# Kernel tuning notes

Hardware: AMD Instinct MI355X
Metric: run time of the kernel (lower is better)

Reference implementation:

```python
import jax, jax.numpy as jnp
import numpy as np

THRESH = 0.5
IOU_THR = 0.3
TOP_K = 512

# standard YOLOv3 anchors for strides 32/16/8 (grids 13/26/52)
ANCHORS_13 = jnp.array([[116., 90.], [156., 198.], [373., 326.]], dtype=jnp.float32)
ANCHORS_26 = jnp.array([[30., 61.], [62., 45.], [59., 119.]], dtype=jnp.float32)
ANCHORS_52 = jnp.array([[10., 13.], [16., 30.], [33., 23.]], dtype=jnp.float32)


def _decode(out, stride, anchors):
    # out: [B, 3*(5+C), H, W] -> [B, H, W, 3, 5+C] (matches permute(0,2,3,1).reshape)
    B, _, H, W = out.shape
    o = jnp.transpose(out, (0, 2, 3, 1)).reshape(B, H, W, 3, -1)
    conf = jax.nn.sigmoid(o[..., 4])          # [B,H,W,3]
    xy = jax.nn.sigmoid(o[..., 0:2])          # sigmoid on x,y as in _filter
    gy = jnp.arange(H, dtype=o.dtype)[None, :, None, None]   # idxs[:,1]
    gx = jnp.arange(W, dtype=o.dtype)[None, None, :, None]   # idxs[:,2]
    cy = (gy + xy[..., 1]) * stride
    cx = (gx + xy[..., 0]) * stride
    w = anchors[:, 0] * jnp.exp(o[..., 2])    # anchors broadcast over anchor dim
    h = anchors[:, 1] * jnp.exp(o[..., 3])
    cls = jnp.argmax(o[..., 5:], axis=-1).astype(o.dtype)
    n = jnp.broadcast_to(jnp.arange(B, dtype=o.dtype)[:, None, None, None], conf.shape)
    w0, h0 = w * 0.5, h * 0.5
    boxes = jnp.stack([conf, cx - w0, cy - h0, cx + w0, cy + h0, cls, n], axis=-1)
    return boxes.reshape(-1, 7), conf.reshape(-1)


def _iou_matrix(b):
    # b: [K,4] = x1,y1,x2,y2 -> [K,K] IoU
    area = jnp.clip(b[:, 2] - b[:, 0], 0) * jnp.clip(b[:, 3] - b[:, 1], 0)
    xx1 = jnp.maximum(b[:, None, 0], b[None, :, 0])
    yy1 = jnp.maximum(b[:, None, 1], b[None, :, 1])
    xx2 = jnp.minimum(b[:, None, 2], b[None, :, 2])
    yy2 = jnp.minimum(b[:, None, 3], b[None, :, 3])
    inter = jnp.clip(xx2 - xx1, 0) * jnp.clip(yy2 - yy1, 0)
    return inter / (area[:, None] + area[None, :] - inter + 1e-9)


def _detect(output_13, output_26, output_52):
    b13, c13 = _decode(output_13, 32.0, ANCHORS_13)
    b26, c26 = _decode(output_26, 16.0, ANCHORS_26)
    b52, c52 = _decode(output_52, 8.0, ANCHORS_52)
    boxes = jnp.concatenate([b13, b26, b52], axis=0)      # [N,7]
    conf = jnp.concatenate([c13, c26, c52], axis=0)       # [N]
    # threshold filter (mask instead of nonzero-compaction for fixed shapes)
    scores = jnp.where(conf > THRESH, conf, 0.0)
    top_scores, idx = jax.lax.top_k(scores, TOP_K)        # sorted descending
    cand = boxes[idx]                                      # [K,7]
    valid = top_scores > THRESH
    iou = _iou_matrix(cand[:, 1:5])
    ar = jnp.arange(TOP_K)

    def body(i, keep):
        sup = keep[i] & (iou[i] > IOU_THR) & (ar > i)
        return keep & ~sup

    keep = jax.lax.fori_loop(0, TOP_K, body, valid)
    # zero out suppressed / invalid rows; rows: [conf, x1, y1, x2, y2, cls, batch]
    return cand * keep[:, None].astype(cand.dtype)


def setup_inputs() -> dict:
    key = jax.random.key(0)
    k1, k2, k3 = jax.random.split(key, 3)
    return {
        "output_13": jax.random.normal(k1, (32, 255, 13, 13), dtype=jnp.float32),
        "output_26": jax.random.normal(k2, (32, 255, 26, 26), dtype=jnp.float32),
        "output_52": jax.random.normal(k3, (32, 255, 52, 52), dtype=jnp.float32),
    }


def reference(output_13, output_26, output_52):
    return _detect(output_13, output_26, output_52)
```

## Files before the change

### kernel.cpp

```cpp
#include <hip/hip_runtime.h>

#define N13E 16224
#define N26E 64896
#define N52E 259584
#define NTOT 340704
#define BASE26 16224
#define BASE52 81120
#define KMAX 2048
#define TOPK 512

__device__ __forceinline__ float sigm(float x) { return 1.0f / (1.0f + expf(-x)); }

__global__ void k_init(unsigned* __restrict__ hist, unsigned* __restrict__ cnt) {
    int t = threadIdx.x;
    for (int i = t; i < 2048; i += 256) hist[i] = 0u;
    if (t == 0) *cnt = 0u;
}

template <int HW>
__device__ __forceinline__ float load_logit(const float* __restrict__ p, int local) {
    int ba = local / HW;
    int hw = local - ba * HW;
    int b = ba / 3;
    int a = ba - b * 3;
    return p[(b * 255 + a * 85 + 4) * HW + hw];
}

__global__ void k_hist(const float* __restrict__ p13, const float* __restrict__ p26,
                       const float* __restrict__ p52, unsigned* __restrict__ hist) {
    int t = blockIdx.x * 256 + threadIdx.x;
    if (t >= NTOT) return;
    float logit;
    if (t < N13E)               logit = load_logit<169>(p13, t);
    else if (t < N13E + N26E)   logit = load_logit<676>(p26, t - N13E);
    else                        logit = load_logit<2704>(p52, t - (N13E + N26E));
    float conf = sigm(logit);
    if (conf > 0.5f) {
        unsigned bin = (__float_as_uint(conf) >> 12) - 0x3F000u;
        bin = (bin > 2047u) ? 2047u : bin;
        atomicAdd(&hist[bin], 1u);
    }
}

__global__ void k_scan(const unsigned* __restrict__ hist, unsigned* __restrict__ thr) {
    __shared__ unsigned tot[256];
    int t = threadIdx.x;
    unsigned loc[8]; unsigned s = 0u;
#pragma unroll
    for (int k = 0; k < 8; ++k) { loc[k] = hist[2047 - (t * 8 + k)]; s += loc[k]; }
    tot[t] = s;
    __syncthreads();
    for (int off = 1; off < 256; off <<= 1) {
        unsigned u = (t >= off) ? tot[t - off] : 0u;
        __syncthreads();
        tot[t] += u;
        __syncthreads();
    }
    unsigned excl = tot[t] - s;
    unsigned total = tot[255];
    if (total < (unsigned)TOPK) {
        if (t == 0) *thr = 0x3F000001u;
    } else {
        unsigned run = excl;
#pragma unroll
        for (int k = 0; k < 8; ++k) {
            unsigned c = run + loc[k];
            if (run < (unsigned)TOPK && c >= (unsigned)TOPK) {
                int bin = 2047 - (t * 8 + k);
                *thr = ((unsigned)(bin + 0x3F000)) << 12;
            }
            run = c;
        }
    }
}

template <int HW, int BASE>
__device__ __forceinline__ void compact_one(const float* __restrict__ p, int local, unsigned thrv,
                                            unsigned* __restrict__ cnt,
                                            unsigned long long* __restrict__ keys) {
    int ba = local / HW;
    int hw = local - ba * HW;
    int b = ba / 3;
    int a = ba - b * 3;
    float logit = p[(b * 255 + a * 85 + 4) * HW + hw];
    float conf = sigm(logit);
    unsigned bits = __float_as_uint(conf);
    if (conf > 0.5f && bits >= thrv) {
        unsigned pos = atomicAdd(cnt, 1u);
        if (pos < (unsigned)KMAX) {
            unsigned concat = (unsigned)(BASE + (b * HW + hw) * 3 + a);
            keys[pos] = (((unsigned long long)bits) << 32) | (unsigned long long)(0xFFFFFFFFu - concat);
        }
    }
}

__global__ void k_compact(const float* __restrict__ p13, const float* __restrict__ p26,
                          const float* __restrict__ p52, const unsigned* __restrict__ thrp,
                          unsigned* __restrict__ cnt, unsigned long long* __restrict__ keys) {
    int t = blockIdx.x * 256 + threadIdx.x;
    if (t >= NTOT) return;
    unsigned thrv = *thrp;
    if (t < N13E)               compact_one<169, 0>(p13, t, thrv, cnt, keys);
    else if (t < N13E + N26E)   compact_one<676, BASE26>(p26, t - N13E, thrv, cnt, keys);
    else                        compact_one<2704, BASE52>(p52, t - (N13E + N26E), thrv, cnt, keys);
}

__global__ void __launch_bounds__(1024) k_sort(const unsigned* __restrict__ cnt,
                                               const unsigned long long* __restrict__ keys,
                                               unsigned long long* __restrict__ sorted) {
    __shared__ unsigned long long sk[KMAX];
    int t = threadIdx.x;
    unsigned n = *cnt; if (n > (unsigned)KMAX) n = (unsigned)KMAX;
    sk[t]        = ((unsigned)t < n)          ? keys[t]        : 0ull;
    sk[t + 1024] = ((unsigned)(t + 1024) < n) ? keys[t + 1024] : 0ull;
    for (unsigned size = 2; size < (unsigned)KMAX; size <<= 1) {
        unsigned ddd = ((t & (int)(size >> 1)) != 0) ? 1u : 0u;
        for (unsigned stride = size >> 1; stride > 0; stride >>= 1) {
            __syncthreads();
            unsigned pos = 2u * (unsigned)t - ((unsigned)t & (stride - 1u));
            unsigned long long a = sk[pos], b = sk[pos + stride];
            if ((unsigned)(a > b) == ddd) { sk[pos] = b; sk[pos + stride] = a; }
        }
    }
    for (unsigned stride = KMAX / 2; stride > 0; stride >>= 1) {
        __syncthreads();
        unsigned pos = 2u * (unsigned)t - ((unsigned)t & (stride - 1u));
        unsigned long long a = sk[pos], b = sk[pos + stride];
        if (a < b) { sk[pos] = b; sk[pos + stride] = a; }
    }
    __syncthreads();
    if (t < TOPK) sorted[t] = sk[t];
}

__device__ __forceinline__ unsigned long long pack_key(float v, int c) {
    unsigned u = __float_as_uint(v);
    unsigned ov = (u & 0x80000000u) ? ~u : (u | 0x80000000u);
    return (((unsigned long long)ov) << 32) | (unsigned long long)(unsigned)(127 - c);
}

template <int HW, int W>
__device__ __forceinline__ void decode_one(const float* __restrict__ p, int local, float strideF,
                                           float aw0, float ah0, float aw1, float ah1, float aw2, float ah2,
                                           float conf, float* __restrict__ outrow, int lane) {
    int a = local % 3;
    int cell = local / 3;
    int b = cell / HW;
    int hw = cell - b * HW;
    int h = hw / W;
    int wc = hw - h * W;
    int cb = b * 255 + a * 85;
    float v1 = p[(cb + 5 + lane) * HW + hw];
    unsigned long long k1 = pack_key(v1, lane);
    if (lane < 16) {
        float v2 = p[(cb + 69 + lane) * HW + hw];
        unsigned long long k2 = pack_key(v2, lane + 64);
        if (k2 > k1) k1 = k2;
    }
#pragma unroll
    for (int m = 32; m >= 1; m >>= 1) {
        unsigned long long o = __shfl_xor(k1, m, 64);
        if (o > k1) k1 = o;
    }
    if (lane == 0) {
        int cls = 127 - (int)(unsigned)(k1 & 0xFFFFFFFFull);
        float t0 = p[(cb + 0) * HW + hw];
        float t1 = p[(cb + 1) * HW + hw];
        float t2 = p[(cb + 2) * HW + hw];
        float t3 = p[(cb + 3) * HW + hw];
        float aw = (a == 0) ? aw0 : ((a == 1) ? aw1 : aw2);
        float ah = (a == 0) ? ah0 : ((a == 1) ? ah1 : ah2);
        float sx = sigm(t0);
        float sy = sigm(t1);
        float bw = aw * expf(t2);
        float bh = ah * expf(t3);
        float cx = ((float)wc + sx) * strideF;
        float cy = ((float)h + sy) * strideF;
        float w0 = bw * 0.5f, h0 = bh * 0.5f;
        outrow[0] = conf;
        outrow[1] = cx - w0;
        outrow[2] = cy - h0;
        outrow[3] = cx + w0;
        outrow[4] = cy + h0;
        outrow[5] = (float)cls;
        outrow[6] = (float)b;
    }
}

__global__ void k_decode(const float* __restrict__ p13, const float* __restrict__ p26,
                         const float* __restrict__ p52, const unsigned long long* __restrict__ sorted,
                         float* __restrict__ cand) {
    int c = blockIdx.x;
    int lane = threadIdx.x;
    unsigned long long key = sorted[c];
    unsigned sb = (unsigned)(key >> 32);
    float* row = cand + c * 7;
    if (sb == 0u) {
        if (lane < 7) row[lane] = 0.0f;
        return;
    }
    unsigned idx = 0xFFFFFFFFu - (unsigned)(key & 0xFFFFFFFFull);
    float conf = __uint_as_float(sb);
    if (idx < N13E)
        decode_one<169, 13>(p13, (int)idx, 32.0f, 116.f, 90.f, 156.f, 198.f, 373.f, 326.f, conf, row, lane);
    else if (idx < N13E + N26E)
        decode_one<676, 26>(p26, (int)idx - BASE26, 16.0f, 30.f, 61.f, 62.f, 45.f, 59.f, 119.f, conf, row, lane);
    else
        decode_one<2704, 52>(p52, (int)idx - BASE52, 8.0f, 10.f, 13.f, 16.f, 30.f, 33.f, 23.f, conf, row, lane);
}

__global__ void k_mask(const float* __restrict__ cand, unsigned long long* __restrict__ mask) {
    int wid = blockIdx.x * blockDim.x + threadIdx.x;
    if (wid >= TOPK * 8) return;
    int i = wid >> 3, jw = wid & 7;
    const float* bi = cand + i * 7;
    float x1 = bi[1], y1 = bi[2], x2 = bi[3], y2 = bi[4];
    float ai = fmaxf(x2 - x1, 0.f) * fmaxf(y2 - y1, 0.f);
    unsigned long long m = 0ull;
    int j0 = jw * 64;
#pragma unroll 4
    for (int bj = 0; bj < 64; ++bj) {
        int j = j0 + bj;
        const float* bjp = cand + j * 7;
        float jx1 = bjp[1], jy1 = bjp[2], jx2 = bjp[3], jy2 = bjp[4];
        float aj = fmaxf(jx2 - jx1, 0.f) * fmaxf(jy2 - jy1, 0.f);
        float xx1 = fmaxf(x1, jx1), yy1 = fmaxf(y1, jy1);
        float xx2 = fminf(x2, jx2), yy2 = fminf(y2, jy2);
        float inter = fmaxf(xx2 - xx1, 0.f) * fmaxf(yy2 - yy1, 0.f);
        float iou = inter / (((ai + aj) - inter) + 1e-9f);
        if ((j > i) && (iou > 0.3f)) m |= (1ull << bj);
    }
    mask[wid] = m;
}

__global__ void __launch_bounds__(512) k_nms(const float* __restrict__ cand,
                                             const unsigned long long* __restrict__ maskg,
                                             float* __restrict__ out) {
    __shared__ unsigned long long smask[TOPK * 8];
    __shared__ unsigned long long live[8];
    __shared__ unsigned long long keepw[8];
    int tid = threadIdx.x;
    for (int p = tid; p < TOPK * 8; p += 512) smask[p] = maskg[p];
    bool validt = cand[tid * 7] > 0.5f;
    unsigned long long bal = __ballot(validt);
    if ((tid & 63) == 0) live[tid >> 6] = bal;
    __syncthreads();
    if (tid < 64) {
        int lane = tid;
        int lw = lane & 7;
        unsigned long long r = 0ull;
#pragma unroll
        for (int w = 0; w < 8; ++w) {
            unsigned long long lvw = live[w];
#pragma unroll 8
            for (int b2 = 0; b2 < 64; ++b2) {
                int i = w * 64 + b2;
                unsigned long long rowv = smask[i * 8 + lw];
                unsigned rlo = (unsigned)__builtin_amdgcn_readlane((int)(unsigned)(r & 0xFFFFFFFFull), w);
                unsigned rhi = (unsigned)__builtin_amdgcn_readlane((int)(unsigned)(r >> 32), w);
                unsigned long long rw = (((unsigned long long)rhi) << 32) | (unsigned long long)rlo;
                bool acc = (((lvw >> b2) & 1ull) != 0ull) && (((rw >> b2) & 1ull) == 0ull);
                if (acc) r |= rowv;
            }
        }
        if (lane < 8) keepw[lane] = live[lane] & ~r;
    }
    __syncthreads();
    for (int p = tid; p < TOPK * 7; p += 512) {
        int i = p / 7;
        unsigned long long kb = (keepw[i >> 6] >> (i & 63)) & 1ull;
        out[p] = kb ? cand[p] : 0.0f;
    }
}

extern "C" void kernel_launch(void* const* d_in, const int* in_sizes, int n_in,
                              void* d_out, int out_size, void* d_ws, size_t ws_size,
                              hipStream_t stream) {
    const float* p13 = (const float*)d_in[0];
    const float* p26 = (const float*)d_in[1];
    const float* p52 = (const float*)d_in[2];
    float* out = (float*)d_out;
    char* ws = (char*)d_ws;

    unsigned* hist             = (unsigned*)(ws + 0);
    unsigned* cnt              = (unsigned*)(ws + 8192);
    unsigned* thr              = (unsigned*)(ws + 8196);
    unsigned long long* keys   = (unsigned long long*)(ws + 8704);
    unsigned long long* sorted = (unsigned long long*)(ws + 25088);
    float* cand                = (float*)(ws + 29184);
    unsigned long long* mask   = (unsigned long long*)(ws + 43520);

    int nb = (NTOT + 255) / 256;
    k_init<<<1, 256, 0, stream>>>(hist, cnt);
    k_hist<<<nb, 256, 0, stream>>>(p13, p26, p52, hist);
    k_scan<<<1, 256, 0, stream>>>(hist, thr);
    k_compact<<<nb, 256, 0, stream>>>(p13, p26, p52, thr, cnt, keys);
    k_sort<<<1, 1024, 0, stream>>>(cnt, keys, sorted);
    k_decode<<<TOPK, 64, 0, stream>>>(p13, p26, p52, sorted, cand);
    k_mask<<<16, 256, 0, stream>>>(cand, mask);
    k_nms<<<1, 512, 0, stream>>>(cand, mask, out);
}
```

Before: 235.7 us.

## Fuse pipeline into three kernels with last-block tails, rank sort, 8-lane decode

```diff
diff --git a/kernel.cpp b/kernel.cpp
--- a/kernel.cpp
+++ b/kernel.cpp
@@ -11,10 +11,10 @@
 
 __device__ __forceinline__ float sigm(float x) { return 1.0f / (1.0f + expf(-x)); }
 
-__global__ void k_init(unsigned* __restrict__ hist, unsigned* __restrict__ cnt) {
-    int t = threadIdx.x;
-    for (int i = t; i < 2048; i += 256) hist[i] = 0u;
-    if (t == 0) *cnt = 0u;
+__device__ __forceinline__ unsigned long long pack_key(float v, int c) {
+    unsigned u = __float_as_uint(v);
+    unsigned ov = (u & 0x80000000u) ? ~u : (u | 0x80000000u);
+    return (((unsigned long long)ov) << 32) | (unsigned long long)(unsigned)(127 - c);
 }
 
 template <int HW>
@@ -26,47 +26,57 @@
     return p[(b * 255 + a * 85 + 4) * HW + hw];
 }
 
-__global__ void k_hist(const float* __restrict__ p13, const float* __restrict__ p26,
-                       const float* __restrict__ p52, unsigned* __restrict__ hist) {
-    int t = blockIdx.x * 256 + threadIdx.x;
-    if (t >= NTOT) return;
-    float logit;
-    if (t < N13E)               logit = load_logit<169>(p13, t);
-    else if (t < N13E + N26E)   logit = load_logit<676>(p26, t - N13E);
-    else                        logit = load_logit<2704>(p52, t - (N13E + N26E));
-    float conf = sigm(logit);
-    if (conf > 0.5f) {
-        unsigned bin = (__float_as_uint(conf) >> 12) - 0x3F000u;
-        bin = (bin > 2047u) ? 2047u : bin;
-        atomicAdd(&hist[bin], 1u);
-    }
-}
-
-__global__ void k_scan(const unsigned* __restrict__ hist, unsigned* __restrict__ thr) {
+__global__ void __launch_bounds__(256) k_hist_scan(const float* __restrict__ p13,
+                                                   const float* __restrict__ p26,
+                                                   const float* __restrict__ p52,
+                                                   unsigned* __restrict__ hist,
+                                                   unsigned* __restrict__ done,
+                                                   unsigned* __restrict__ thr) {
     __shared__ unsigned tot[256];
-    int t = threadIdx.x;
+    __shared__ unsigned amLast;
+    int tid = threadIdx.x;
+    int t = blockIdx.x * 256 + tid;
+    if (t < NTOT) {
+        float logit;
+        if (t < N13E)               logit = load_logit<169>(p13, t);
+        else if (t < N13E + N26E)   logit = load_logit<676>(p26, t - N13E);
+        else                        logit = load_logit<2704>(p52, t - (N13E + N26E));
+        float conf = sigm(logit);
+        if (conf > 0.5f) {
+            unsigned bin = (__float_as_uint(conf) >> 12) - 0x3F000u;
+            bin = (bin > 2047u) ? 2047u : bin;
+            atomicAdd(&hist[bin], 1u);
+        }
+    }
+    __threadfence();
+    __syncthreads();
+    if (tid == 0) amLast = (atomicAdd(done, 1u) == gridDim.x - 1) ? 1u : 0u;
+    __syncthreads();
+    if (!amLast) return;
+    __threadfence();
+
     unsigned loc[8]; unsigned s = 0u;
 #pragma unroll
-    for (int k = 0; k < 8; ++k) { loc[k] = hist[2047 - (t * 8 + k)]; s += loc[k]; }
-    tot[t] = s;
+    for (int k = 0; k < 8; ++k) { loc[k] = hist[2047 - (tid * 8 + k)]; s += loc[k]; }
+    tot[tid] = s;
     __syncthreads();
     for (int off = 1; off < 256; off <<= 1) {
-        unsigned u = (t >= off) ? tot[t - off] : 0u;
+        unsigned u = (tid >= off) ? tot[tid - off] : 0u;
         __syncthreads();
-        tot[t] += u;
+        tot[tid] += u;
         __syncthreads();
     }
-    unsigned excl = tot[t] - s;
+    unsigned excl = tot[tid] - s;
     unsigned total = tot[255];
     if (total < (unsigned)TOPK) {
-        if (t == 0) *thr = 0x3F000001u;
+        if (tid == 0) *thr = 0x3F000001u;
     } else {
         unsigned run = excl;
 #pragma unroll
         for (int k = 0; k < 8; ++k) {
             unsigned c = run + loc[k];
             if (run < (unsigned)TOPK && c >= (unsigned)TOPK) {
-                int bin = 2047 - (t * 8 + k);
+                int bin = 2047 - (tid * 8 + k);
                 *thr = ((unsigned)(bin + 0x3F000)) << 12;
             }
             run = c;
@@ -94,54 +104,57 @@
     }
 }
 
-__global__ void k_compact(const float* __restrict__ p13, const float* __restrict__ p26,
-                          const float* __restrict__ p52, const unsigned* __restrict__ thrp,
-                          unsigned* __restrict__ cnt, unsigned long long* __restrict__ keys) {
-    int t = blockIdx.x * 256 + threadIdx.x;
-    if (t >= NTOT) return;
-    unsigned thrv = *thrp;
-    if (t < N13E)               compact_one<169, 0>(p13, t, thrv, cnt, keys);
-    else if (t < N13E + N26E)   compact_one<676, BASE26>(p26, t - N13E, thrv, cnt, keys);
-    else                        compact_one<2704, BASE52>(p52, t - (N13E + N26E), thrv, cnt, keys);
-}
-
-__global__ void __launch_bounds__(1024) k_sort(const unsigned* __restrict__ cnt,
-                                               const unsigned long long* __restrict__ keys,
-                                               unsigned long long* __restrict__ sorted) {
-    __shared__ unsigned long long sk[KMAX];
-    int t = threadIdx.x;
+__global__ void __launch_bounds__(512) k_compact_rank(const float* __restrict__ p13,
+                                                      const float* __restrict__ p26,
+                                                      const float* __restrict__ p52,
+                                                      const unsigned* __restrict__ thrp,
+                                                      unsigned* __restrict__ cnt,
+                                                      unsigned long long* __restrict__ keys,
+                                                      unsigned* __restrict__ done,
+                                                      unsigned long long* __restrict__ sorted) {
+    __shared__ unsigned long long keysL[KMAX];
+    __shared__ unsigned long long sortedL[TOPK];
+    __shared__ unsigned amLast;
+    int tid = threadIdx.x;
+    int t = blockIdx.x * 512 + tid;
+    if (t < NTOT) {
+        unsigned thrv = *thrp;
+        if (t < N13E)               compact_one<169, 0>(p13, t, thrv, cnt, keys);
+        else if (t < N13E + N26E)   compact_one<676, BASE26>(p26, t - N13E, thrv, cnt, keys);
+        else                        compact_one<2704, BASE52>(p52, t - (N13E + N26E), thrv, cnt, keys);
+    }
+    __threadfence();
+    __syncthreads();
+    if (tid == 0) amLast = (atomicAdd(done, 1u) == gridDim.x - 1) ? 1u : 0u;
+    __syncthreads();
+    if (!amLast) return;
+    __threadfence();
+
     unsigned n = *cnt; if (n > (unsigned)KMAX) n = (unsigned)KMAX;
-    sk[t]        = ((unsigned)t < n)          ? keys[t]        : 0ull;
-    sk[t + 1024] = ((unsigned)(t + 1024) < n) ? keys[t + 1024] : 0ull;
-    for (unsigned size = 2; size < (unsigned)KMAX; size <<= 1) {
-        unsigned ddd = ((t & (int)(size >> 1)) != 0) ? 1u : 0u;
-        for (unsigned stride = size >> 1; stride > 0; stride >>= 1) {
-            __syncthreads();
-            unsigned pos = 2u * (unsigned)t - ((unsigned)t & (stride - 1u));
-            unsigned long long a = sk[pos], b = sk[pos + stride];
-            if ((unsigned)(a > b) == ddd) { sk[pos] = b; sk[pos + stride] = a; }
-        }
-    }
-    for (unsigned stride = KMAX / 2; stride > 0; stride >>= 1) {
-        __syncthreads();
-        unsigned pos = 2u * (unsigned)t - ((unsigned)t & (stride - 1u));
-        unsigned long long a = sk[pos], b = sk[pos + stride];
-        if (a < b) { sk[pos] = b; sk[pos + stride] = a; }
-    }
-    __syncthreads();
-    if (t < TOPK) sorted[t] = sk[t];
-}
-
-__device__ __forceinline__ unsigned long long pack_key(float v, int c) {
-    unsigned u = __float_as_uint(v);
-    unsigned ov = (u & 0x80000000u) ? ~u : (u | 0x80000000u);
-    return (((unsigned long long)ov) << 32) | (unsigned long long)(unsigned)(127 - c);
+    for (int j = tid; j < (int)n; j += 512) keysL[j] = keys[j];
+    sortedL[tid] = 0ull;
+    __syncthreads();
+
+    unsigned long long mine[4]; unsigned rk[4]; int nown = 0;
+#pragma unroll
+    for (int k = 0; k < 4; ++k) {
+        int idx = tid + k * 512;
+        if (idx < (int)n) { mine[nown] = keysL[idx]; rk[nown] = 0u; ++nown; }
+    }
+    for (int j = 0; j < (int)n; ++j) {
+        unsigned long long kj = keysL[j];
+        for (int m = 0; m < nown; ++m) rk[m] += (kj > mine[m]) ? 1u : 0u;
+    }
+    for (int m = 0; m < nown; ++m)
+        if (rk[m] < (unsigned)TOPK) sortedL[rk[m]] = mine[m];
+    __syncthreads();
+    sorted[tid] = sortedL[tid];
 }
 
 template <int HW, int W>
-__device__ __forceinline__ void decode_one(const float* __restrict__ p, int local, float strideF,
-                                           float aw0, float ah0, float aw1, float ah1, float aw2, float ah2,
-                                           float conf, float* __restrict__ outrow, int lane) {
+__device__ __forceinline__ void decode8(const float* __restrict__ p, int local, float strideF,
+                                        float aw0, float ah0, float aw1, float ah1, float aw2, float ah2,
+                                        float conf, float* __restrict__ outrow, int l) {
     int a = local % 3;
     int cell = local / 3;
     int b = cell / HW;
@@ -149,19 +162,21 @@
     int h = hw / W;
     int wc = hw - h * W;
     int cb = b * 255 + a * 85;
-    float v1 = p[(cb + 5 + lane) * HW + hw];
-    unsigned long long k1 = pack_key(v1, lane);
-    if (lane < 16) {
-        float v2 = p[(cb + 69 + lane) * HW + hw];
-        unsigned long long k2 = pack_key(v2, lane + 64);
-        if (k2 > k1) k1 = k2;
-    }
-#pragma unroll
-    for (int m = 32; m >= 1; m >>= 1) {
+    float v0 = p[(cb + 5 + l) * HW + hw];
+    unsigned long long k1 = pack_key(v0, l);
+#pragma unroll
+    for (int k = 1; k < 10; ++k) {
+        int c = l + 8 * k;
+        float v = p[(cb + 5 + c) * HW + hw];
+        unsigned long long kk = pack_key(v, c);
+        if (kk > k1) k1 = kk;
+    }
+#pragma unroll
+    for (int m = 4; m >= 1; m >>= 1) {
         unsigned long long o = __shfl_xor(k1, m, 64);
         if (o > k1) k1 = o;
     }
-    if (lane == 0) {
+    if (l == 0) {
         int cls = 127 - (int)(unsigned)(k1 & 0xFFFFFFFFull);
         float t0 = p[(cb + 0) * HW + hw];
         float t1 = p[(cb + 1) * HW + hw];
@@ -186,64 +201,81 @@
     }
 }
 
-__global__ void k_decode(const float* __restrict__ p13, const float* __restrict__ p26,
-                         const float* __restrict__ p52, const unsigned long long* __restrict__ sorted,
-                         float* __restrict__ cand) {
-    int c = blockIdx.x;
-    int lane = threadIdx.x;
-    unsigned long long key = sorted[c];
+__global__ void __launch_bounds__(512) k_decode_mask_nms(const float* __restrict__ p13,
+                                                         const float* __restrict__ p26,
+                                                         const float* __restrict__ p52,
+                                                         const unsigned long long* __restrict__ sorted,
+                                                         float* __restrict__ cand,
+                                                         unsigned* __restrict__ done,
+                                                         float* __restrict__ out) {
+    __shared__ float cx1[TOPK], cy1[TOPK], cx2[TOPK], cy2[TOPK], car[TOPK], cco[TOPK];
+    __shared__ unsigned long long smask[TOPK * 8];
+    __shared__ unsigned long long live[8], keepw[8];
+    __shared__ unsigned amLast;
+    int tid = threadIdx.x;
+
+    int box = blockIdx.x * 64 + (tid >> 3);
+    int l = tid & 7;
+    unsigned long long key = sorted[box];
     unsigned sb = (unsigned)(key >> 32);
-    float* row = cand + c * 7;
+    float* row = cand + box * 7;
     if (sb == 0u) {
-        if (lane < 7) row[lane] = 0.0f;
-        return;
-    }
-    unsigned idx = 0xFFFFFFFFu - (unsigned)(key & 0xFFFFFFFFull);
-    float conf = __uint_as_float(sb);
-    if (idx < N13E)
-        decode_one<169, 13>(p13, (int)idx, 32.0f, 116.f, 90.f, 156.f, 198.f, 373.f, 326.f, conf, row, lane);
-    else if (idx < N13E + N26E)
-        decode_one<676, 26>(p26, (int)idx - BASE26, 16.0f, 30.f, 61.f, 62.f, 45.f, 59.f, 119.f, conf, row, lane);
-    else
-        decode_one<2704, 52>(p52, (int)idx - BASE52, 8.0f, 10.f, 13.f, 16.f, 30.f, 33.f, 23.f, conf, row, lane);
-}
-
-__global__ void k_mask(const float* __restrict__ cand, unsigned long long* __restrict__ mask) {
-    int wid = blockIdx.x * blockDim.x + threadIdx.x;
-    if (wid >= TOPK * 8) return;
-    int i = wid >> 3, jw = wid & 7;
-    const float* bi = cand + i * 7;
-    float x1 = bi[1], y1 = bi[2], x2 = bi[3], y2 = bi[4];
-    float ai = fmaxf(x2 - x1, 0.f) * fmaxf(y2 - y1, 0.f);
-    unsigned long long m = 0ull;
-    int j0 = jw * 64;
-#pragma unroll 4
-    for (int bj = 0; bj < 64; ++bj) {
-        int j = j0 + bj;
-        const float* bjp = cand + j * 7;
-        float jx1 = bjp[1], jy1 = bjp[2], jx2 = bjp[3], jy2 = bjp[4];
-        float aj = fmaxf(jx2 - jx1, 0.f) * fmaxf(jy2 - jy1, 0.f);
-        float xx1 = fmaxf(x1, jx1), yy1 = fmaxf(y1, jy1);
-        float xx2 = fminf(x2, jx2), yy2 = fminf(y2, jy2);
-        float inter = fmaxf(xx2 - xx1, 0.f) * fmaxf(yy2 - yy1, 0.f);
-        float iou = inter / (((ai + aj) - inter) + 1e-9f);
-        if ((j > i) && (iou > 0.3f)) m |= (1ull << bj);
-    }
-    mask[wid] = m;
-}
-
-__global__ void __launch_bounds__(512) k_nms(const float* __restrict__ cand,
-                                             const unsigned long long* __restrict__ maskg,
-                                             float* __restrict__ out) {
-    __shared__ unsigned long long smask[TOPK * 8];
-    __shared__ unsigned long long live[8];
-    __shared__ unsigned long long keepw[8];
-    int tid = threadIdx.x;
-    for (int p = tid; p < TOPK * 8; p += 512) smask[p] = maskg[p];
-    bool validt = cand[tid * 7] > 0.5f;
+        if (l < 7) row[l] = 0.0f;
+    } else {
+        unsigned idx = 0xFFFFFFFFu - (unsigned)(key & 0xFFFFFFFFull);
+        float conf = __uint_as_float(sb);
+        if (idx < N13E)
+            decode8<169, 13>(p13, (int)idx, 32.0f, 116.f, 90.f, 156.f, 198.f, 373.f, 326.f, conf, row, l);
+        else if (idx < N13E + N26E)
+            decode8<676, 26>(p26, (int)idx - BASE26, 16.0f, 30.f, 61.f, 62.f, 45.f, 59.f, 119.f, conf, row, l);
+        else
+            decode8<2704, 52>(p52, (int)idx - BASE52, 8.0f, 10.f, 13.f, 16.f, 30.f, 33.f, 23.f, conf, row, l);
+    }
+    __threadfence();
+    __syncthreads();
+    if (tid == 0) amLast = (atomicAdd(done, 1u) == gridDim.x - 1) ? 1u : 0u;
+    __syncthreads();
+    if (!amLast) return;
+    __threadfence();
+
+    {
+        int p = tid;
+        float c0 = cand[p * 7 + 0];
+        float x1 = cand[p * 7 + 1], y1 = cand[p * 7 + 2];
+        float x2 = cand[p * 7 + 3], y2 = cand[p * 7 + 4];
+        cco[p] = c0; cx1[p] = x1; cy1[p] = y1; cx2[p] = x2; cy2[p] = y2;
+        car[p] = fmaxf(x2 - x1, 0.f) * fmaxf(y2 - y1, 0.f);
+    }
+    __syncthreads();
+
+    {
+        int i = tid;
+        float x1 = cx1[i], y1 = cy1[i], x2 = cx2[i], y2 = cy2[i];
+        float ai = car[i];
+#pragma unroll
+        for (int jw = 0; jw < 8; ++jw) {
+            unsigned long long m = 0ull;
+            int j0 = jw * 64;
+            if (i < j0 + 63) {
+                for (int bj = 0; bj < 64; ++bj) {
+                    int j = j0 + bj;
+                    float jx1 = cx1[j], jy1 = cy1[j], jx2 = cx2[j], jy2 = cy2[j];
+                    float aj = car[j];
+                    float xx1 = fmaxf(x1, jx1), yy1 = fmaxf(y1, jy1);
+                    float xx2 = fminf(x2, jx2), yy2 = fminf(y2, jy2);
+                    float inter = fmaxf(xx2 - xx1, 0.f) * fmaxf(yy2 - yy1, 0.f);
+                    float iou = inter / (((ai + aj) - inter) + 1e-9f);
+                    if ((j > i) && (iou > 0.3f)) m |= (1ull << bj);
+                }
+            }
+            smask[i * 8 + jw] = m;
+        }
+    }
+    bool validt = cco[tid] > 0.5f;
     unsigned long long bal = __ballot(validt);
     if ((tid & 63) == 0) live[tid >> 6] = bal;
     __syncthreads();
+
     if (tid < 64) {
         int lane = tid;
         int lw = lane & 7;
@@ -265,6 +297,7 @@
         if (lane < 8) keepw[lane] = live[lane] & ~r;
     }
     __syncthreads();
+
     for (int p = tid; p < TOPK * 7; p += 512) {
         int i = p / 7;
         unsigned long long kb = (keepw[i >> 6] >> (i & 63)) & 1ull;
@@ -283,19 +316,19 @@
 
     unsigned* hist             = (unsigned*)(ws + 0);
     unsigned* cnt              = (unsigned*)(ws + 8192);
-    unsigned* thr              = (unsigned*)(ws + 8196);
+    unsigned* done1            = (unsigned*)(ws + 8196);
+    unsigned* done2            = (unsigned*)(ws + 8200);
+    unsigned* done3            = (unsigned*)(ws + 8204);
+    unsigned* thr              = (unsigned*)(ws + 8208);
     unsigned long long* keys   = (unsigned long long*)(ws + 8704);
     unsigned long long* sorted = (unsigned long long*)(ws + 25088);
     float* cand                = (float*)(ws + 29184);
-    unsigned long long* mask   = (unsigned long long*)(ws + 43520);
-
-    int nb = (NTOT + 255) / 256;
-    k_init<<<1, 256, 0, stream>>>(hist, cnt);
-    k_hist<<<nb, 256, 0, stream>>>(p13, p26, p52, hist);
-    k_scan<<<1, 256, 0, stream>>>(hist, thr);
-    k_compact<<<nb, 256, 0, stream>>>(p13, p26, p52, thr, cnt, keys);
-    k_sort<<<1, 1024, 0, stream>>>(cnt, keys, sorted);
-    k_decode<<<TOPK, 64, 0, stream>>>(p13, p26, p52, sorted, cand);
-    k_mask<<<16, 256, 0, stream>>>(cand, mask);
-    k_nms<<<1, 512, 0, stream>>>(cand, mask, out);
-}
+
+    hipMemsetAsync(ws, 0, 8208, stream);
+
+    int gh = (NTOT + 255) / 256;
+    int gc = (NTOT + 511) / 512;
+    k_hist_scan<<<gh, 256, 0, stream>>>(p13, p26, p52, hist, done1, thr);
+    k_compact_rank<<<gc, 512, 0, stream>>>(p13, p26, p52, thr, cnt, keys, done2, sorted);
+    k_decode_mask_nms<<<8, 512, 0, stream>>>(p13, p26, p52, sorted, cand, done3, out);
+}
```

Measured after the change: 490.3 us. 2.08x slower.
